# Kernel optimization log

Hardware: AMD Instinct MI355X
Metric: run time of the kernel (lower is better)

## Reference

```python
import jax, jax.numpy as jnp
import numpy as np

N = 12288      # nodes
E = 393216     # edges (avg degree 32)
IN = 256       # in_channels
HID = 128      # hidden_channels
H = 4          # nheads (conv1)
OUT = 64       # out_channels
NEG_SLOPE = 0.2


def setup_inputs() -> dict:
    key = jax.random.key(0)
    ks = jax.random.split(key, 12)
    def g(k, shape, fan):
        return (jax.random.normal(k, shape, jnp.float32) / np.sqrt(fan)).astype(jnp.float32)
    x = jax.random.normal(ks[0], (N, IN), jnp.float32)
    edge_index = jax.random.randint(ks[1], (2, E), 0, N, dtype=jnp.int32)
    # GATConv layer 1: shared lin for src/dst, per-head attention vectors, bias
    W1 = g(ks[2], (IN, H * HID), IN)
    att_src1 = g(ks[3], (H, HID), HID)
    att_dst1 = g(ks[4], (H, HID), HID)
    b1 = jnp.zeros((H * HID,), jnp.float32)
    # GATConv layer 2: heads=1, concat=False
    W2 = g(ks[5], (H * HID, OUT), H * HID)
    att_src2 = g(ks[6], (1, OUT), OUT)
    att_dst2 = g(ks[7], (1, OUT), OUT)
    b2 = jnp.zeros((OUT,), jnp.float32)
    # final Linear(out_channels, in_channels * stack_num)
    Wl = g(ks[8], (OUT, IN), OUT)
    bl = jnp.zeros((IN,), jnp.float32)
    return {"x": x, "edge_index": edge_index, "W1": W1, "att_src1": att_src1,
            "att_dst1": att_dst1, "b1": b1, "W2": W2, "att_src2": att_src2,
            "att_dst2": att_dst2, "b2": b2, "Wl": Wl, "bl": bl}


def gat_layer(x, W, att_src, att_dst, bias, src, dst, concat):
    """PyG GATConv (v1), eval mode (no dropout), self-loops already in src/dst."""
    n = x.shape[0]
    Hh, C = att_src.shape
    h = (x @ W).reshape(n, Hh, C)                       # [N,H,C]
    a_src = jnp.einsum('nhc,hc->nh', h, att_src)        # [N,H]
    a_dst = jnp.einsum('nhc,hc->nh', h, att_dst)
    e = jax.nn.leaky_relu(a_src[src] + a_dst[dst], NEG_SLOPE)  # [E,H]
    # segment softmax over edges grouped by destination node
    m = jax.ops.segment_max(e, dst, num_segments=n)     # [N,H]
    e = jnp.exp(e - m[dst])
    denom = jax.ops.segment_sum(e, dst, num_segments=n)
    alpha = e / (denom[dst] + 1e-16)                    # [E,H]
    msg = h[src] * alpha[:, :, None]                    # [E,H,C]
    out = jax.ops.segment_sum(msg, dst, num_segments=n) # [N,H,C]
    out = out.reshape(n, Hh * C) if concat else out.mean(axis=1)
    return out + bias


def reference(x, edge_index, W1, att_src1, att_dst1, b1, W2, att_src2, att_dst2, b2, Wl, bl):
    n = x.shape[0]
    loop = jnp.arange(n, dtype=edge_index.dtype)
    src = jnp.concatenate([edge_index[0], loop])  # add_self_loops=True (PyG default)
    dst = jnp.concatenate([edge_index[1], loop])
    h = gat_layer(x, W1, att_src1, att_dst1, b1, src, dst, concat=True)   # [N, H*HID]
    h = gat_layer(h, W2, att_src2, att_dst2, b2, src, dst, concat=False)  # [N, OUT]
    # F.normalize(h, p=2, dim=1)
    z = h / jnp.maximum(jnp.linalg.norm(h, axis=1, keepdims=True), 1e-12)
    x_ = jax.nn.elu(z @ Wl + bl)                   # [N, IN]
    A_pred = jax.nn.sigmoid(z @ z.T)               # [N, N]
    return A_pred, z, x_
```

## Files before the change

### kernel.cpp

```cpp
#include <hip/hip_runtime.h>
#include <hip/hip_bf16.h>

#define NNODES 12288
#define NEDGES 393216
#define ETOT   (NEDGES + NNODES)
#define INCH   256
#define HIDC   128
#define NH     4
#define HC     512
#define OUTC   64
#define SLOPE  0.2f

__device__ __forceinline__ float leaky(float v){ return v > 0.f ? v : SLOPE*v; }

__device__ __forceinline__ float wave_sum(float v){
#pragma unroll
  for (int m=32;m>0;m>>=1) v += __shfl_xor(v, m);
  return v;
}
__device__ __forceinline__ float wave_max(float v){
#pragma unroll
  for (int m=32;m>0;m>>=1) v = fmaxf(v, __shfl_xor(v, m));
  return v;
}

template<int EPI, bool BT>
__global__ __launch_bounds__(256) void gemm64(
    const float* __restrict__ A, const float* __restrict__ B,
    const float* __restrict__ bias, float* __restrict__ C,
    int M, int K, int Nc)
{
  __shared__ float As[16][68];
  __shared__ float Bs[16][68];
  int t = threadIdx.x;
  int tx = t & 15, ty = t >> 4;
  int m0 = blockIdx.y * 64, n0 = blockIdx.x * 64;
  float acc[4][4] = {};
  for (int k0 = 0; k0 < K; k0 += 16) {
    {
      int m = t >> 2, kk = (t & 3) << 2;
      const float4 v = *(const float4*)&A[(size_t)(m0+m)*K + k0 + kk];
      As[kk+0][m] = v.x; As[kk+1][m] = v.y; As[kk+2][m] = v.z; As[kk+3][m] = v.w;
    }
    if (!BT) {
      int kk = t >> 4, nn = (t & 15) << 2;
      *(float4*)&Bs[kk][nn] = *(const float4*)&B[(size_t)(k0+kk)*Nc + n0 + nn];
    } else {
      int nn = t >> 2, kk = (t & 3) << 2;
      const float4 v = *(const float4*)&B[(size_t)(n0+nn)*K + k0 + kk];
      Bs[kk+0][nn] = v.x; Bs[kk+1][nn] = v.y; Bs[kk+2][nn] = v.z; Bs[kk+3][nn] = v.w;
    }
    __syncthreads();
#pragma unroll
    for (int kk = 0; kk < 16; ++kk) {
      float4 a = *(const float4*)&As[kk][ty<<2];
      float4 b = *(const float4*)&Bs[kk][tx<<2];
      float av[4]={a.x,a.y,a.z,a.w}, bv[4]={b.x,b.y,b.z,b.w};
#pragma unroll
      for (int i=0;i<4;++i)
#pragma unroll
        for (int j=0;j<4;++j) acc[i][j] += av[i]*bv[j];
    }
    __syncthreads();
  }
#pragma unroll
  for (int i=0;i<4;++i) {
    int row = m0 + (ty<<2) + i;
    int col = n0 + (tx<<2);
    float4 o; float* po = &o.x;
#pragma unroll
    for (int j=0;j<4;++j) {
      float v = acc[i][j];
      if (EPI==1) v += bias[col+j];
      if (EPI==2) { v += bias[col+j]; v = v>0.f ? v : (__expf(v)-1.f); }
      if (EPI==3) { v = 1.f/(1.f+__expf(-v)); }
      po[j]=v;
    }
    *(float4*)&C[(size_t)row*Nc + col] = o;
  }
}

__global__ __launch_bounds__(256) void att1_kernel(
  const float* __restrict__ h1, const float* __restrict__ att_src,
  const float* __restrict__ att_dst, float* __restrict__ as1, float* __restrict__ ad1)
{
  int n = blockIdx.x; int t = threadIdx.x; int h = t>>6, lane = t&63;
  float2 v = *(const float2*)&h1[(size_t)n*HC + h*HIDC + lane*2];
  float2 a = *(const float2*)&att_src[h*HIDC + lane*2];
  float2 b = *(const float2*)&att_dst[h*HIDC + lane*2];
  float ps = wave_sum(v.x*a.x + v.y*a.y);
  float pd = wave_sum(v.x*b.x + v.y*b.y);
  if (lane==0){ as1[n*NH+h]=ps; ad1[n*NH+h]=pd; }
}

__global__ void zero_ints(int* p, int n){ int i=blockIdx.x*256+threadIdx.x; if(i<n) p[i]=0; }

__global__ void hist_kernel(const int* __restrict__ ei_dst, int* __restrict__ cnt){
  int e = blockIdx.x*256+threadIdx.x;
  if (e >= ETOT) return;
  int dst = e < NEDGES ? ei_dst[e] : e - NEDGES;
  atomicAdd(&cnt[dst], 1);
}

__global__ __launch_bounds__(1024) void scan_kernel(const int* __restrict__ cnt,
    int* __restrict__ rowptr, int* __restrict__ nxt){
  __shared__ int part[1024];
  int tid = threadIdx.x;
  int c[12]; int s=0;
  int base = tid*12;
#pragma unroll
  for (int j=0;j<12;++j){ c[j]=cnt[base+j]; s+=c[j]; }
  part[tid]=s; __syncthreads();
  for (int off=1; off<1024; off<<=1){
    int v=0; if (tid>=off) v=part[tid-off];
    __syncthreads();
    part[tid]+=v;
    __syncthreads();
  }
  int run = part[tid]-s;
#pragma unroll
  for (int j=0;j<12;++j){ rowptr[base+j]=run; nxt[base+j]=run; run+=c[j]; }
  if (tid==1023) rowptr[NNODES]=run;
}

__global__ void scatter_kernel(const int* __restrict__ ei_dst, int* __restrict__ nxt,
                               int* __restrict__ eids){
  int e = blockIdx.x*256+threadIdx.x;
  if (e >= ETOT) return;
  int dst = e < NEDGES ? ei_dst[e] : e - NEDGES;
  int pos = atomicAdd(&nxt[dst], 1);
  eids[pos] = e;
}

__global__ __launch_bounds__(256) void agg1_kernel(
  const float* __restrict__ h1, const float* __restrict__ as1, const float* __restrict__ ad1,
  const int* __restrict__ rowptr, const int* __restrict__ eids, const int* __restrict__ ei_src,
  const float* __restrict__ b1, float* __restrict__ out)
{
  __shared__ float4 red[256];
  int n = blockIdx.x; int t = threadIdx.x;
  int s0 = rowptr[n], s1 = rowptr[n+1];
  float ad[4];
#pragma unroll
  for (int h=0;h<4;++h) ad[h]=ad1[n*NH+h];
  float mx[4]={-1e30f,-1e30f,-1e30f,-1e30f};
  for (int i=s0+t;i<s1;i+=256){
    int eid=eids[i]; int src = eid<NEDGES ? ei_src[eid] : eid-NEDGES;
#pragma unroll
    for (int h=0;h<4;++h){ float v=leaky(as1[src*NH+h]+ad[h]); mx[h]=fmaxf(mx[h],v); }
  }
  red[t]=make_float4(mx[0],mx[1],mx[2],mx[3]); __syncthreads();
  for (int off=128;off>0;off>>=1){
    if (t<off){ float4 a=red[t], b=red[t+off];
      red[t]=make_float4(fmaxf(a.x,b.x),fmaxf(a.y,b.y),fmaxf(a.z,b.z),fmaxf(a.w,b.w)); }
    __syncthreads();
  }
  float4 M4 = red[0]; __syncthreads();
  float mm[4]={M4.x,M4.y,M4.z,M4.w};
  float sm[4]={0.f,0.f,0.f,0.f};
  for (int i=s0+t;i<s1;i+=256){
    int eid=eids[i]; int src = eid<NEDGES ? ei_src[eid] : eid-NEDGES;
#pragma unroll
    for (int h=0;h<4;++h){ float v=leaky(as1[src*NH+h]+ad[h]); sm[h]+=__expf(v-mm[h]); }
  }
  red[t]=make_float4(sm[0],sm[1],sm[2],sm[3]); __syncthreads();
  for (int off=128;off>0;off>>=1){
    if (t<off){ float4 a=red[t], b=red[t+off];
      red[t]=make_float4(a.x+b.x,a.y+b.y,a.z+b.z,a.w+b.w); }
    __syncthreads();
  }
  float4 S4 = red[0];
  float rden[4]={1.f/(S4.x+1e-16f),1.f/(S4.y+1e-16f),1.f/(S4.z+1e-16f),1.f/(S4.w+1e-16f)};
  int w = t>>6, lane = t&63;
  float adw=ad[w], mw=mm[w], rw=rden[w];
  float2 acc = make_float2(0.f,0.f);
  for (int i=s0;i<s1;++i){
    int eid=eids[i]; int src = eid<NEDGES ? ei_src[eid] : eid-NEDGES;
    float v = leaky(as1[src*NH+w]+adw);
    float alpha = __expf(v-mw)*rw;
    float2 hv = *(const float2*)&h1[(size_t)src*HC + w*HIDC + lane*2];
    acc.x += alpha*hv.x; acc.y += alpha*hv.y;
  }
  float2 bb = *(const float2*)&b1[w*HIDC + lane*2];
  *(float2*)&out[(size_t)n*HC + w*HIDC + lane*2] = make_float2(acc.x+bb.x, acc.y+bb.y);
}

__global__ __launch_bounds__(256) void att2_kernel(const float* __restrict__ h2a,
  const float* __restrict__ att_src, const float* __restrict__ att_dst,
  float* __restrict__ as2, float* __restrict__ ad2)
{
  int t=threadIdx.x; int lane=t&63;
  int n = blockIdx.x*4 + (t>>6);
  float v = h2a[(size_t)n*OUTC + lane];
  float ps = wave_sum(v*att_src[lane]);
  float pd = wave_sum(v*att_dst[lane]);
  if (lane==0){ as2[n]=ps; ad2[n]=pd; }
}

__global__ __launch_bounds__(64) void agg2_kernel(const float* __restrict__ h2a,
  const float* __restrict__ as2, const float* __restrict__ ad2,
  const int* __restrict__ rowptr, const int* __restrict__ eids, const int* __restrict__ ei_src,
  const float* __restrict__ b2, float* __restrict__ z)
{
  int n = blockIdx.x; int lane = threadIdx.x;
  int s0 = rowptr[n], s1 = rowptr[n+1];
  float adn = ad2[n];
  float mx = -1e30f;
  for (int i=s0+lane;i<s1;i+=64){
    int eid=eids[i]; int src = eid<NEDGES ? ei_src[eid] : eid-NEDGES;
    mx = fmaxf(mx, leaky(as2[src]+adn));
  }
  mx = wave_max(mx);
  float sm = 0.f;
  for (int i=s0+lane;i<s1;i+=64){
    int eid=eids[i]; int src = eid<NEDGES ? ei_src[eid] : eid-NEDGES;
    sm += __expf(leaky(as2[src]+adn)-mx);
  }
  sm = wave_sum(sm);
  float rden = 1.f/(sm+1e-16f);
  float acc = 0.f;
  for (int i=s0;i<s1;++i){
    int eid=eids[i]; int src = eid<NEDGES ? ei_src[eid] : eid-NEDGES;
    float alpha = __expf(leaky(as2[src]+adn)-mx)*rden;
    acc += alpha * h2a[(size_t)src*OUTC + lane];
  }
  float o = acc + b2[lane];
  float nrm2 = wave_sum(o*o);
  float nrm = sqrtf(nrm2);
  z[(size_t)n*OUTC + lane] = o / fmaxf(nrm, 1e-12f);
}

extern "C" void kernel_launch(void* const* d_in, const int* in_sizes, int n_in,
                              void* d_out, int out_size, void* d_ws, size_t ws_size,
                              hipStream_t stream)
{
  const float* x        = (const float*)d_in[0];
  const int*   ei       = (const int*)d_in[1];
  const float* W1       = (const float*)d_in[2];
  const float* att_src1 = (const float*)d_in[3];
  const float* att_dst1 = (const float*)d_in[4];
  const float* b1       = (const float*)d_in[5];
  const float* W2       = (const float*)d_in[6];
  const float* att_src2 = (const float*)d_in[7];
  const float* att_dst2 = (const float*)d_in[8];
  const float* b2       = (const float*)d_in[9];
  const float* Wl       = (const float*)d_in[10];
  const float* bl       = (const float*)d_in[11];
  const int* ei_src = ei;
  const int* ei_dst = ei + NEDGES;

  float* Apred = (float*)d_out;
  float* z     = Apred + (size_t)NNODES*NNODES;
  float* x_    = z + (size_t)NNODES*OUTC;

  const size_t NEED =
      ((size_t)NNODES*HC*4   + 256) +
      ((size_t)NNODES*HC*4   + 256) +
      ((size_t)NNODES*OUTC*4 + 256) +
      ((size_t)NNODES*NH*4   + 256) * 2 +
      ((size_t)NNODES*4      + 256) * 2 +
      ((size_t)(NNODES+1)*4  + 256) +
      ((size_t)NNODES*4      + 256) * 2 +
      ((size_t)ETOT*4        + 256);
  char* base = (ws_size >= NEED) ? (char*)d_ws : (char*)Apred;
  size_t o = 0;
  auto alloc = [&](size_t bytes){ void* p = base + o; o += (bytes + 255) & ~(size_t)255; return p; };
  float* h1    = (float*)alloc((size_t)NNODES*HC*4);
  float* h1agg = (float*)alloc((size_t)NNODES*HC*4);
  float* h2a   = (float*)alloc((size_t)NNODES*OUTC*4);
  float* as1   = (float*)alloc((size_t)NNODES*NH*4);
  float* ad1   = (float*)alloc((size_t)NNODES*NH*4);
  float* as2   = (float*)alloc((size_t)NNODES*4);
  float* ad2   = (float*)alloc((size_t)NNODES*4);
  int* rowptr  = (int*)alloc((NNODES+1)*4);
  int* cnt     = (int*)alloc((size_t)NNODES*4);
  int* nxt     = (int*)alloc((size_t)NNODES*4);
  int* eids    = (int*)alloc((size_t)ETOT*4);

  zero_ints<<<(NNODES+255)/256,256,0,stream>>>(cnt, NNODES);
  hist_kernel<<<(ETOT+255)/256,256,0,stream>>>(ei_dst, cnt);
  scan_kernel<<<1,1024,0,stream>>>(cnt, rowptr, nxt);
  scatter_kernel<<<(ETOT+255)/256,256,0,stream>>>(ei_dst, nxt, eids);

  dim3 g1(HC/64, NNODES/64);
  gemm64<0,false><<<g1,256,0,stream>>>(x, W1, nullptr, h1, NNODES, INCH, HC);
  att1_kernel<<<NNODES,256,0,stream>>>(h1, att_src1, att_dst1, as1, ad1);
  agg1_kernel<<<NNODES,256,0,stream>>>(h1, as1, ad1, rowptr, eids, ei_src, b1, h1agg);

  dim3 g2(OUTC/64, NNODES/64);
  gemm64<0,false><<<g2,256,0,stream>>>(h1agg, W2, nullptr, h2a, NNODES, HC, OUTC);
  att2_kernel<<<NNODES/4,256,0,stream>>>(h2a, att_src2, att_dst2, as2, ad2);
  agg2_kernel<<<NNODES,64,0,stream>>>(h2a, as2, ad2, rowptr, eids, ei_src, b2, z);

  dim3 g3(INCH/64, NNODES/64);
  gemm64<2,false><<<g3,256,0,stream>>>(z, Wl, bl, x_, NNODES, OUTC, INCH);

  dim3 g4(NNODES/64, NNODES/64);
  gemm64<3,true><<<g4,256,0,stream>>>(z, z, nullptr, Apred, NNODES, OUTC, NNODES);
}
```

Baseline: 1.186 ms.

## Compute A_pred with bf16 MFMA kernel using swizzled shared-memory tiles

Replaces the fp32 SIMT gemm for sigmoid(z z^T) with a dedicated MFMA kernel. Each block converts 128x64 tiles of z to bf16 in XOR-swizzled LDS and runs 16x16x32 bf16 MFMAs, then applies the sigmoid and stores to the 12288x12288 output. This targets the compute cost of the largest GEMM. The risk is bf16 precision loss in the dot products, and the output store pattern (16 consecutive floats per row per lane group) may be less coalesced than the old float4 stores.

```diff
diff --git a/kernel.cpp b/kernel.cpp
--- a/kernel.cpp
+++ b/kernel.cpp
@@ -11,7 +11,16 @@
 #define OUTC   64
 #define SLOPE  0.2f
 
+typedef __attribute__((ext_vector_type(8))) short bf16x8;
+typedef __attribute__((ext_vector_type(4))) float f32x4;
+
 __device__ __forceinline__ float leaky(float v){ return v > 0.f ? v : SLOPE*v; }
+
+__device__ __forceinline__ short bf16cvt(float f){
+  union { float f; unsigned u; } x; x.f = f;
+  unsigned r = (x.u + 0x7fffu + ((x.u >> 16) & 1u)) >> 16;
+  return (short)r;
+}
 
 __device__ __forceinline__ float wave_sum(float v){
 #pragma unroll
@@ -78,6 +87,74 @@
     }
     *(float4*)&C[(size_t)row*Nc + col] = o;
   }
+}
+
+__global__ __launch_bounds__(256) void apred_mfma(
+    const float* __restrict__ z, float* __restrict__ A)
+{
+  __shared__ short As[128*64];
+  __shared__ short Bs[128*64];
+  int t = threadIdx.x;
+  int m0 = blockIdx.y * 128, n0 = blockIdx.x * 128;
+#pragma unroll
+  for (int i = 0; i < 4; ++i) {
+    int c = t + 256*i;
+    int row = c >> 3, col8 = c & 7;
+    int addr = row*128 + ((col8*16) ^ ((row & 7) << 4));
+    {
+      const float4* p = (const float4*)&z[(size_t)(m0+row)*OUTC + col8*8];
+      float4 v0 = p[0], v1 = p[1];
+      bf16x8 pk = { bf16cvt(v0.x), bf16cvt(v0.y), bf16cvt(v0.z), bf16cvt(v0.w),
+                    bf16cvt(v1.x), bf16cvt(v1.y), bf16cvt(v1.z), bf16cvt(v1.w) };
+      *(bf16x8*)((char*)As + addr) = pk;
+    }
+    {
+      const float4* p = (const float4*)&z[(size_t)(n0+row)*OUTC + col8*8];
+      float4 v0 = p[0], v1 = p[1];
+      bf16x8 pk = { bf16cvt(v0.x), bf16cvt(v0.y), bf16cvt(v0.z), bf16cvt(v0.w),
+                    bf16cvt(v1.x), bf16cvt(v1.y), bf16cvt(v1.z), bf16cvt(v1.w) };
+      *(bf16x8*)((char*)Bs + addr) = pk;
+    }
+  }
+  __syncthreads();
+  int w = t >> 6, lane = t & 63;
+  int wr = (w >> 1) * 64, wc = (w & 1) * 64;
+  int lr = lane & 15, lk = lane >> 4;
+  bf16x8 af[4][2], bf[4][2];
+#pragma unroll
+  for (int f = 0; f < 4; ++f)
+#pragma unroll
+    for (int kk = 0; kk < 2; ++kk) {
+      int ra = wr + f*16 + lr;
+      int rb = wc + f*16 + lr;
+      int colb = (kk*64 + lk*16);
+      af[f][kk] = *(const bf16x8*)((char*)As + ra*128 + (colb ^ ((ra & 7) << 4)));
+      bf[f][kk] = *(const bf16x8*)((char*)Bs + rb*128 + (colb ^ ((rb & 7) << 4)));
+    }
+  f32x4 acc[4][4];
+#pragma unroll
+  for (int i=0;i<4;++i)
+#pragma unroll
+    for (int j=0;j<4;++j) acc[i][j] = (f32x4){0.f,0.f,0.f,0.f};
+#pragma unroll
+  for (int kk = 0; kk < 2; ++kk)
+#pragma unroll
+    for (int mi = 0; mi < 4; ++mi)
+#pragma unroll
+      for (int nj = 0; nj < 4; ++nj)
+        acc[mi][nj] = __builtin_amdgcn_mfma_f32_16x16x32_bf16(af[mi][kk], bf[nj][kk], acc[mi][nj], 0, 0, 0);
+#pragma unroll
+  for (int mi = 0; mi < 4; ++mi)
+#pragma unroll
+    for (int nj = 0; nj < 4; ++nj) {
+      int row = m0 + wr + mi*16 + lk*4;
+      int col = n0 + wc + nj*16 + lr;
+#pragma unroll
+      for (int r = 0; r < 4; ++r) {
+        float v = acc[mi][nj][r];
+        A[(size_t)(row + r) * NNODES + col] = 1.f/(1.f + __expf(-v));
+      }
+    }
 }
 
 __global__ __launch_bounds__(256) void att1_kernel(
@@ -295,6 +372,6 @@
   dim3 g3(INCH/64, NNODES/64);
   gemm64<2,false><<<g3,256,0,stream>>>(z, Wl, bl, x_, NNODES, OUTC, INCH);
 
-  dim3 g4(NNODES/64, NNODES/64);
-  gemm64<3,true><<<g4,256,0,stream>>>(z, z, nullptr, Apred, NNODES, OUTC, NNODES);
-}
+  dim3 g4(NNODES/128, NNODES/128);
+  apred_mfma<<<g4,256,0,stream>>>(z, Apred);
+}
```

Result: faster. 1.010 ms (-14.9%).
